# Kernel optimization log

Measured on AMD Instinct MI355X. Metric: run time of the kernel, lower is better.

## Reference

```python
import jax, jax.numpy as jnp
import numpy as np
import math

D_MODEL = 512
N_HEADS = 8
D_K = D_MODEL // N_HEADS
D_FF = 2048
EPS = 1e-6


def _layer_norm(x, gamma, beta):
    # Matches the torch module: unbiased std (ddof=1), divide by (std + eps)
    mean = jnp.mean(x, axis=-1, keepdims=True)
    std = jnp.std(x, axis=-1, ddof=1, keepdims=True)
    return gamma * (x - mean) / (std + EPS) + beta


def setup_inputs() -> dict:
    key = jax.random.key(0)
    ks = jax.random.split(key, 16)
    B, S = 4, 2048
    s_attn = 1.0 / math.sqrt(D_MODEL)
    s_ff1 = 1.0 / math.sqrt(D_MODEL)
    s_ff2 = 1.0 / math.sqrt(D_FF)
    inp = {
        "x": jax.random.normal(ks[0], (B, S, D_MODEL), dtype=jnp.float32),
        "mask": jnp.ones((1, 1, S, S), dtype=jnp.int32),
        "wq": jax.random.normal(ks[1], (D_MODEL, D_MODEL), jnp.float32) * s_attn,
        "bq": jnp.zeros((D_MODEL,), jnp.float32),
        "wk": jax.random.normal(ks[2], (D_MODEL, D_MODEL), jnp.float32) * s_attn,
        "bk": jnp.zeros((D_MODEL,), jnp.float32),
        "wv": jax.random.normal(ks[3], (D_MODEL, D_MODEL), jnp.float32) * s_attn,
        "bv": jnp.zeros((D_MODEL,), jnp.float32),
        "wo": jax.random.normal(ks[4], (D_MODEL, D_MODEL), jnp.float32) * s_attn,
        "bo": jnp.zeros((D_MODEL,), jnp.float32),
        "w1": jax.random.normal(ks[5], (D_MODEL, D_FF), jnp.float32) * s_ff1,
        "b1": jnp.zeros((D_FF,), jnp.float32),
        "w2": jax.random.normal(ks[6], (D_FF, D_MODEL), jnp.float32) * s_ff2,
        "b2": jnp.zeros((D_MODEL,), jnp.float32),
        "g1": jnp.ones((1, 1, D_MODEL), jnp.float32),
        "be1": jnp.zeros((1, 1, D_MODEL), jnp.float32),
        "g2": jnp.ones((1, 1, D_MODEL), jnp.float32),
        "be2": jnp.zeros((1, 1, D_MODEL), jnp.float32),
    }
    return inp


def reference(x, mask, wq, bq, wk, bk, wv, bv, wo, bo, w1, b1, w2, b2, g1, be1, g2, be2):
    B, S, _ = x.shape
    # --- residual 1: pre-norm self-attention ---
    xn = _layer_norm(x, g1, be1)
    q = (xn @ wq + bq).reshape(B, S, N_HEADS, D_K).transpose(0, 2, 1, 3)
    k = (xn @ wk + bk).reshape(B, S, N_HEADS, D_K).transpose(0, 2, 1, 3)
    v = (xn @ wv + bv).reshape(B, S, N_HEADS, D_K).transpose(0, 2, 1, 3)
    # NOTE: source uses floor division `//` by sqrt(d_k) (a faithful-ly kept bug)
    scores = jnp.floor_divide(jnp.einsum("bhqd,bhkd->bhqk", q, k), math.sqrt(D_K))
    scores = jnp.where(mask == 0, jnp.float32(-1e9), scores)
    attn = jax.nn.softmax(scores, axis=-1)
    ctx = jnp.einsum("bhqk,bhkd->bhqd", attn, v)
    ctx = ctx.transpose(0, 2, 1, 3).reshape(B, S, D_MODEL)
    x = x + (ctx @ wo + bo)
    # --- residual 2: pre-norm feed-forward ---
    xn2 = _layer_norm(x, g2, be2)
    ff = jax.nn.relu(xn2 @ w1 + b1) @ w2 + b2
    return x + ff
```

## Files before the change

kernel.cpp:

```cpp
#include <hip/hip_runtime.h>
#include <cmath>

#define SEQ 2048
#define DM 512
#define DFF 2048
#define NH 8
#define DKH 64
#define NROWS 8192

typedef __attribute__((ext_vector_type(8))) short bf16x8;
typedef __attribute__((ext_vector_type(16))) float f32x16;

__device__ __forceinline__ ushort f2bf(float f) {
    uint u = __float_as_uint(f);
    u += 0x7fff + ((u >> 16) & 1);
    return (ushort)(u >> 16);
}
__device__ __forceinline__ float bf2f(ushort h) {
    return __uint_as_float(((uint)h) << 16);
}
__device__ __forceinline__ uint cvtpk_bf16(float a, float b) {
    uint r;
    asm("v_cvt_pk_bf16_f32 %0, %1, %2" : "=v"(r) : "v"(a), "v"(b));
    return r;
}
__device__ __forceinline__ void gl_lds16(const void* g, void* l) {
    __builtin_amdgcn_global_load_lds(
        (const __attribute__((address_space(1))) void*)g,
        (__attribute__((address_space(3))) void*)l, 16, 0, 0);
}
__device__ __forceinline__ void* swz(char* base, int row, int col) {
    int byte = (row << 7) + (col << 1);
    byte ^= (row & 7) << 4;
    return base + byte;
}
__device__ __forceinline__ void* swzg(char* base, int row, int k) {
    int byte = (row << 7) + (k << 1);
    byte ^= ((row >> 2) & 7) << 4;
    return base + byte;
}

template<bool SPLIT>
__global__ __launch_bounds__(64) void ln_kernel(const float* __restrict__ x,
        const float* __restrict__ g, const float* __restrict__ b,
        ushort* __restrict__ oh, ushort* __restrict__ ol) {
    int row = blockIdx.x;
    int t = threadIdx.x;
    const float* xr = x + (size_t)row * DM + t * 8;
    float v[8];
    *(float4*)&v[0] = *(const float4*)(xr);
    *(float4*)&v[4] = *(const float4*)(xr + 4);
    float s = 0.f;
    #pragma unroll
    for (int j = 0; j < 8; ++j) s += v[j];
    #pragma unroll
    for (int m = 32; m > 0; m >>= 1) s += __shfl_xor(s, m);
    float mean = s * (1.0f / DM);
    float ss = 0.f;
    #pragma unroll
    for (int j = 0; j < 8; ++j) { float d = v[j] - mean; ss += d * d; }
    #pragma unroll
    for (int m = 32; m > 0; m >>= 1) ss += __shfl_xor(ss, m);
    float inv = 1.0f / (sqrtf(ss * (1.0f / (DM - 1))) + 1e-6f);
    float gv[8], bv[8];
    *(float4*)&gv[0] = *(const float4*)(g + t * 8);
    *(float4*)&gv[4] = *(const float4*)(g + t * 8 + 4);
    *(float4*)&bv[0] = *(const float4*)(b + t * 8);
    *(float4*)&bv[4] = *(const float4*)(b + t * 8 + 4);
    union { ushort us[8]; float4 f4; } ph, pl;
    #pragma unroll
    for (int j = 0; j < 8; ++j) {
        float o = gv[j] * (v[j] - mean) * inv + bv[j];
        ushort hb = f2bf(o);
        ph.us[j] = hb;
        if (SPLIT) pl.us[j] = f2bf(o - bf2f(hb));
    }
    *(float4*)(oh + (size_t)row * DM + t * 8) = ph.f4;
    if (SPLIT) *(float4*)(ol + (size_t)row * DM + t * 8) = pl.f4;
}

__global__ __launch_bounds__(256) void wconv4(
        const float* __restrict__ wq, const float* __restrict__ wk,
        const float* __restrict__ wv, const float* __restrict__ wo,
        ushort* __restrict__ qh, ushort* __restrict__ ql,
        ushort* __restrict__ kh, ushort* __restrict__ kl,
        ushort* __restrict__ vh, ushort* __restrict__ oh) {
    const int K = DM, N = DM;
    __shared__ float tile[64][65];
    int z = blockIdx.z;
    const float* W = (z == 0) ? wq : (z == 1) ? wk : (z == 2) ? wv : wo;
    ushort* Th = (z == 0) ? qh : (z == 1) ? kh : (z == 2) ? vh : oh;
    ushort* Tl = (z == 0) ? ql : (z == 1) ? kl : nullptr;
    bool split = (z < 2);
    int k0 = blockIdx.x * 64, n0 = blockIdx.y * 64;
    int t = threadIdx.x;
    {
        int kr = t >> 2, c0 = (t & 3) * 16;
        const float* src = W + (size_t)(k0 + kr) * N + n0 + c0;
        #pragma unroll
        for (int j = 0; j < 4; ++j)
            *(float4*)&tile[kr][c0 + j * 4] = *(const float4*)(src + j * 4);
    }
    __syncthreads();
    int n = t >> 2, kc = (t & 3) * 16;
    union { ushort us[16]; float4 f4[2]; } ph, pl;
    #pragma unroll
    for (int j = 0; j < 16; ++j) {
        float v = tile[kc + j][n];
        ushort hb = f2bf(v);
        ph.us[j] = hb;
        pl.us[j] = f2bf(v - bf2f(hb));
    }
    ushort* dh = Th + (size_t)(n0 + n) * K + k0 + kc;
    *(float4*)(dh) = ph.f4[0];
    *(float4*)(dh + 8) = ph.f4[1];
    if (split) {
        ushort* dl = Tl + (size_t)(n0 + n) * K + k0 + kc;
        *(float4*)(dl) = pl.f4[0];
        *(float4*)(dl + 8) = pl.f4[1];
    }
}

__global__ __launch_bounds__(256) void wconv(const float* __restrict__ W,
        ushort* __restrict__ Th, int K, int N) {
    __shared__ float tile[64][65];
    int k0 = blockIdx.x * 64, n0 = blockIdx.y * 64;
    int t = threadIdx.x;
    {
        int kr = t >> 2, c0 = (t & 3) * 16;
        const float* src = W + (size_t)(k0 + kr) * N + n0 + c0;
        #pragma unroll
        for (int j = 0; j < 4; ++j)
            *(float4*)&tile[kr][c0 + j * 4] = *(const float4*)(src + j * 4);
    }
    __syncthreads();
    int n = t >> 2, kc = (t & 3) * 16;
    union { ushort us[16]; float4 f4[2]; } ph;
    #pragma unroll
    for (int j = 0; j < 16; ++j) ph.us[j] = f2bf(tile[kc + j][n]);
    ushort* dh = Th + (size_t)(n0 + n) * K + k0 + kc;
    *(float4*)(dh) = ph.f4[0];
    *(float4*)(dh + 8) = ph.f4[1];
}

__global__ __launch_bounds__(256) void vtrans(const ushort* __restrict__ vh,
        ushort* __restrict__ vt) {
    __shared__ __align__(16) char tile[8192];
    int s0 = blockIdx.x * 64;
    int bh = blockIdx.y;
    int b = bh >> 3, h = bh & 7;
    int t = threadIdx.x;
    {
        int r = t >> 2, co = (t & 3) * 16;
        const ushort* src = vh + (size_t)(b * SEQ + s0 + r) * DM + h * DKH + co;
        *(float4*)swz(tile, r, co) = *(const float4*)(src);
        *(float4*)swz(tile, r, co + 8) = *(const float4*)(src + 8);
    }
    __syncthreads();
    int d = t >> 2, j0 = (t & 3) * 16;
    union { ushort us[16]; float4 f4[2]; } o;
    #pragma unroll
    for (int j = 0; j < 16; ++j)
        o.us[j] = *(ushort*)swz(tile, j0 + j, d);
    ushort* dst = vt + ((size_t)bh * DKH + d) * SEQ + s0 + j0;
    *(float4*)(dst) = o.f4[0];
    *(float4*)(dst + 8) = o.f4[1];
}

__global__ __launch_bounds__(64) void maskprep(const int* __restrict__ mask,
        ushort* __restrict__ mb, unsigned char* __restrict__ mflag) {
    int row = blockIdx.x;
    int lane = threadIdx.x;
    ushort neg = f2bf(-1e9f);
    unsigned long long bal[4];
    #pragma unroll
    for (int u = 0; u < 4; ++u) {
        int base = row * SEQ + u * 512 + lane * 8;
        int4 a = *(const int4*)(mask + base);
        int4 c = *(const int4*)(mask + base + 4);
        union { ushort us[8]; float4 f4; } o;
        o.us[0] = a.x ? (ushort)0 : neg;
        o.us[1] = a.y ? (ushort)0 : neg;
        o.us[2] = a.z ? (ushort)0 : neg;
        o.us[3] = a.w ? (ushort)0 : neg;
        o.us[4] = c.x ? (ushort)0 : neg;
        o.us[5] = c.y ? (ushort)0 : neg;
        o.us[6] = c.z ? (ushort)0 : neg;
        o.us[7] = c.w ? (ushort)0 : neg;
        *(float4*)(mb + base) = o.f4;
        bool ok = a.x && a.y && a.z && a.w && c.x && c.y && c.z && c.w;
        bal[u] = __ballot(ok);
    }
    if (lane < 32) {
        int u = lane >> 3;
        unsigned long long bsel = bal[0];
        bsel = (u == 1) ? bal[1] : bsel;
        bsel = (u == 2) ? bal[2] : bsel;
        bsel = (u == 3) ? bal[3] : bsel;
        int byte = (int)((bsel >> ((lane & 7) * 8)) & 0xFFull);
        mflag[row * 32 + lane] = (byte == 0xFF) ? 1 : 0;
    }
}

template<bool RELU, bool HASRES, int OUT>
__global__ __launch_bounds__(256) void mgemm(
        const ushort* __restrict__ Ah, const ushort* __restrict__ Bth,
        const float* __restrict__ bias, const float* __restrict__ resid,
        float* __restrict__ Cf, ushort* __restrict__ Cbh,
        int M, int N, int K) {
    __shared__ __align__(16) char smem[65536];
    int tid = threadIdx.x;
    int lane = tid & 63, w = tid >> 6;
    int ln31 = lane & 31, hi = lane >> 5;
    int mh = (w >> 1) * 64, nh = (w & 1) * 64;
    int gx = gridDim.x;
    int nwg = gx * gridDim.y;
    int flat = blockIdx.y * gx + blockIdx.x;
    int sid = (flat & 7) * (nwg >> 3) + (flat >> 3);
    int n0 = (sid % gx) * 128;
    int m0 = (sid / gx) * 128;

    f32x16 acc[2][2];
    #pragma unroll
    for (int i = 0; i < 2; ++i)
        #pragma unroll
        for (int j = 0; j < 2; ++j)
            #pragma unroll
            for (int r = 0; r < 16; ++r) acc[i][j][r] = 0.f;

    auto stage = [&](char* Abuf, char* Bbuf, int k0) {
        #pragma unroll
        for (int c = 0; c < 4; ++c) {
            int ch = w * 4 + c;
            int r = ch * 8 + (lane >> 3);
            int u = (lane & 7) ^ ((r >> 2) & 7);
            gl_lds16(Ah + (size_t)(m0 + r) * K + k0 + u * 8, Abuf + ch * 1024);
            gl_lds16(Bth + (size_t)(n0 + r) * K + k0 + u * 8, Bbuf + ch * 1024);
        }
    };

    char* A0 = smem;
    char* B0 = smem + 16384;
    char* A1 = smem + 32768;
    char* B1 = smem + 49152;

    stage(A0, B0, 0);
    __syncthreads();
    int nk = K / 64;
    for (int kt = 0; kt < nk; ++kt) {
        char* Ac = (kt & 1) ? A1 : A0;
        char* Bc = (kt & 1) ? B1 : B0;
        if (kt + 1 < nk)
            stage((kt & 1) ? A0 : A1, (kt & 1) ? B0 : B1, (kt + 1) * 64);
        __builtin_amdgcn_s_setprio(1);
        #pragma unroll
        for (int km = 0; km < 4; ++km) {
            int kk = km * 16 + hi * 8;
            bf16x8 ah[2], bh[2];
            ah[0] = *(bf16x8*)swzg(Ac, mh + ln31, kk);
            ah[1] = *(bf16x8*)swzg(Ac, mh + 32 + ln31, kk);
            bh[0] = *(bf16x8*)swzg(Bc, nh + ln31, kk);
            bh[1] = *(bf16x8*)swzg(Bc, nh + 32 + ln31, kk);
            #pragma unroll
            for (int mi = 0; mi < 2; ++mi)
                #pragma unroll
                for (int ni = 0; ni < 2; ++ni)
                    acc[mi][ni] = __builtin_amdgcn_mfma_f32_32x32x16_bf16(
                        ah[mi], bh[ni], acc[mi][ni], 0, 0, 0);
        }
        __builtin_amdgcn_s_setprio(0);
        __syncthreads();
    }
    float bv[2];
    bv[0] = bias[n0 + nh + ln31];
    bv[1] = bias[n0 + nh + 32 + ln31];
    #pragma unroll
    for (int mi = 0; mi < 2; ++mi)
        #pragma unroll
        for (int ni = 0; ni < 2; ++ni) {
            int n = n0 + nh + ni * 32 + ln31;
            #pragma unroll
            for (int r = 0; r < 16; ++r) {
                int m = m0 + mh + mi * 32 + (r & 3) + 8 * (r >> 2) + 4 * hi;
                float v = acc[mi][ni][r] + bv[ni];
                if (HASRES) v += resid[(size_t)m * N + n];
                if (RELU) v = fmaxf(v, 0.f);
                size_t idx = (size_t)m * N + n;
                if (OUT == 0) Cf[idx] = v;
                else Cbh[idx] = f2bf(v);
            }
        }
}

__global__ __launch_bounds__(256) void qkv_gemm(
        const ushort* __restrict__ Ah, const ushort* __restrict__ Al,
        const ushort* __restrict__ Bth, const ushort* __restrict__ Btl,
        const float* __restrict__ bq, const float* __restrict__ bk,
        const float* __restrict__ bv_, ushort* __restrict__ q_h,
        ushort* __restrict__ q_l, ushort* __restrict__ k_h,
        ushort* __restrict__ k_l, ushort* __restrict__ v_h) {
    const int K = DM, N = DM;
    __shared__ __align__(16) char smem[65536];
    char* As_h = smem;
    char* Bs_h = smem + 16384;
    char* As_l = smem + 32768;
    char* Bs_l = smem + 49152;
    int tid = threadIdx.x;
    int lane = tid & 63, w = tid >> 6;
    int ln31 = lane & 31, hi = lane >> 5;
    int mh = (w >> 1) * 64, nh = (w & 1) * 64;
    int gx = gridDim.x;
    int nwg = gx * gridDim.y;
    int flat = blockIdx.y * gx + blockIdx.x;
    int sid = (flat & 7) * (nwg >> 3) + (flat >> 3);
    int n0 = (sid % gx) * 128;
    int m0 = (sid / gx) * 128;
    bool isqk = (n0 < 1024);

    f32x16 acc[2][2];
    #pragma unroll
    for (int i = 0; i < 2; ++i)
        #pragma unroll
        for (int j = 0; j < 2; ++j)
            #pragma unroll
            for (int r = 0; r < 16; ++r) acc[i][j][r] = 0.f;

    for (int k0 = 0; k0 < K; k0 += 64) {
        #pragma unroll
        for (int c = 0; c < 4; ++c) {
            int ch = w * 4 + c;
            int r = ch * 8 + (lane >> 3);
            int u = (lane & 7) ^ ((r >> 2) & 7);
            gl_lds16(Ah + (size_t)(m0 + r) * K + k0 + u * 8, As_h + ch * 1024);
            gl_lds16(Bth + (size_t)(n0 + r) * K + k0 + u * 8, Bs_h + ch * 1024);
            if (isqk) {
                gl_lds16(Al + (size_t)(m0 + r) * K + k0 + u * 8, As_l + ch * 1024);
                gl_lds16(Btl + (size_t)(n0 + r) * K + k0 + u * 8, Bs_l + ch * 1024);
            }
        }
        __syncthreads();
        __builtin_amdgcn_s_setprio(1);
        #pragma unroll
        for (int km = 0; km < 4; ++km) {
            int kk = km * 16 + hi * 8;
            bf16x8 ah[2], bh[2];
            ah[0] = *(bf16x8*)swzg(As_h, mh + ln31, kk);
            ah[1] = *(bf16x8*)swzg(As_h, mh + 32 + ln31, kk);
            bh[0] = *(bf16x8*)swzg(Bs_h, nh + ln31, kk);
            bh[1] = *(bf16x8*)swzg(Bs_h, nh + 32 + ln31, kk);
            if (isqk) {
                bf16x8 al[2], bl[2];
                al[0] = *(bf16x8*)swzg(As_l, mh + ln31, kk);
                al[1] = *(bf16x8*)swzg(As_l, mh + 32 + ln31, kk);
                bl[0] = *(bf16x8*)swzg(Bs_l, nh + ln31, kk);
                bl[1] = *(bf16x8*)swzg(Bs_l, nh + 32 + ln31, kk);
                #pragma unroll
                for (int mi = 0; mi < 2; ++mi)
                    #pragma unroll
                    for (int ni = 0; ni < 2; ++ni) {
                        acc[mi][ni] = __builtin_amdgcn_mfma_f32_32x32x16_bf16(
                            ah[mi], bh[ni], acc[mi][ni], 0, 0, 0);
                        acc[mi][ni] = __builtin_amdgcn_mfma_f32_32x32x16_bf16(
                            ah[mi], bl[ni], acc[mi][ni], 0, 0, 0);
                        acc[mi][ni] = __builtin_amdgcn_mfma_f32_32x32x16_bf16(
                            al[mi], bh[ni], acc[mi][ni], 0, 0, 0);
                    }
            } else {
                #pragma unroll
                for (int mi = 0; mi < 2; ++mi)
                    #pragma unroll
                    for (int ni = 0; ni < 2; ++ni)
                        acc[mi][ni] = __builtin_amdgcn_mfma_f32_32x32x16_bf16(
                            ah[mi], bh[ni], acc[mi][ni], 0, 0, 0);
            }
        }
        __builtin_amdgcn_s_setprio(0);
        __syncthreads();
    }
    const float* bias = (n0 < 512) ? bq : (n0 < 1024 ? bk : bv_);
    int ncol0 = n0 & 511;
    ushort* Oh = (n0 < 512) ? q_h : (n0 < 1024 ? k_h : v_h);
    ushort* Ol = (n0 < 512) ? q_l : (n0 < 1024 ? k_l : nullptr);
    float scale = (n0 < 512) ? 0.125f : 1.0f;
    float bvv[2];
    bvv[0] = bias[ncol0 + nh + ln31];
    bvv[1] = bias[ncol0 + nh + 32 + ln31];
    #pragma unroll
    for (int mi = 0; mi < 2; ++mi)
        #pragma unroll
        for (int ni = 0; ni < 2; ++ni) {
            int n = ncol0 + nh + ni * 32 + ln31;
            #pragma unroll
            for (int r = 0; r < 16; ++r) {
                int m = m0 + mh + mi * 32 + (r & 3) + 8 * (r >> 2) + 4 * hi;
                float v = (acc[mi][ni][r] + bvv[ni]) * scale;
                size_t idx = (size_t)m * N + n;
                ushort hb = f2bf(v);
                Oh[idx] = hb;
                if (isqk) Ol[idx] = f2bf(v - bf2f(hb));
            }
        }
}

__global__ __launch_bounds__(256, 3) void attn_kernel(
        const ushort* __restrict__ Qh, const ushort* __restrict__ Ql,
        const ushort* __restrict__ Khg, const ushort* __restrict__ Klg,
        const ushort* __restrict__ Vtg, const ushort* __restrict__ mb,
        const unsigned char* __restrict__ mflag,
        ushort* __restrict__ pctx0, ushort* __restrict__ pctx1,
        float2* __restrict__ ml) {
    __shared__ __align__(16) char smem[40960];
    int tid = threadIdx.x;
    int w = tid >> 6, lane = tid & 63;
    int ln31 = lane & 31, hi = lane >> 5;
    bool hib = (hi != 0);
    int f = blockIdx.y * gridDim.x + blockIdx.x;
    int g = (f & 7) * 128 + (f >> 3);
    int bh = g >> 5, rest = g & 31;
    int part = rest >> 4, qb = rest & 15;
    int b = bh >> 3, h = bh & 7;
    int q0 = qb * 128;
    size_t brow = (size_t)b * SEQ;
    int hcol = h * DKH;
    int ktbeg = part * 16, ktend = ktbeg + 16;

    auto stage_K = [&](int kt) {
        char* buf = smem + (kt & 1) * 16384;
        #pragma unroll
        for (int c = 0; c < 2; ++c) {
            int ch = w * 2 + c;
            int r = ch * 8 + (lane >> 3);
            int u = (lane & 7) ^ (r & 7);
            gl_lds16(Khg + (brow + kt * 64 + r) * DM + hcol + u * 8,
                     buf + ch * 1024);
            gl_lds16(Klg + (brow + kt * 64 + r) * DM + hcol + u * 8,
                     buf + 8192 + ch * 1024);
        }
    };
    auto stage_V = [&](int kt) {
        char* buf = smem + 32768;
        #pragma unroll
        for (int c = 0; c < 2; ++c) {
            int ch = w * 2 + c;
            int r = ch * 8 + (lane >> 3);
            int u = (lane & 7) ^ (r & 7);
            gl_lds16(Vtg + ((size_t)bh * DKH + r) * SEQ + kt * 64 + u * 8,
                     buf + ch * 1024);
        }
    };

    {
        char* QhL = smem;
        char* QlL = smem + 16384;
        #pragma unroll
        for (int c = 0; c < 4; ++c) {
            int ch = w * 4 + c;
            int r = ch * 8 + (lane >> 3);
            int u = (lane & 7) ^ (r & 7);
            gl_lds16(Qh + (brow + q0 + r) * DM + hcol + u * 8, QhL + ch * 1024);
            gl_lds16(Ql + (brow + q0 + r) * DM + hcol + u * 8, QlL + ch * 1024);
        }
    }
    __syncthreads();
    bf16x8 qfh[4], qfl[4];
    {
        int qr = w * 32 + ln31;
        #pragma unroll
        for (int c = 0; c < 4; ++c) {
            qfh[c] = *(bf16x8*)swz(smem, qr, c * 16 + hi * 8);
            qfl[c] = *(bf16x8*)swz(smem + 16384, qr, c * 16 + hi * 8);
        }
    }
    __syncthreads();
    stage_K(ktbeg);
    stage_V(ktbeg);
    __syncthreads();

    f32x16 ctx0, ctx1;
    #pragma unroll
    for (int r = 0; r < 16; ++r) { ctx0[r] = 0.f; ctx1[r] = 0.f; }
    float m_i = -1e30f, l_i = 0.f;
    int qglob = q0 + w * 32 + ln31;
    const ushort* mrow = mb + (size_t)qglob * SEQ;

    for (int kt = ktbeg; kt < ktend; ++kt) {
        if (kt + 1 < ktend) stage_K(kt + 1);
        char* KhL = smem + (kt & 1) * 16384;
        char* KlL = KhL + 8192;
        char* VtL = smem + 32768;
        unsigned char fl = mflag[qglob * 32 + kt];
        bool domask = !__all(fl != 0);
        ushort4 mpre[8];
        if (domask) {
            #pragma unroll
            for (int i = 0; i < 8; ++i)
                mpre[i] = *(const ushort4*)(mrow + kt * 64 + i * 8 + hi * 4);
        }
        #pragma unroll
        for (int ksub = 0; ksub < 2; ++ksub) {
            f32x16 s;
            #pragma unroll
            for (int r = 0; r < 16; ++r) s[r] = 0.f;
            __builtin_amdgcn_s_setprio(1);
            #pragma unroll
            for (int c = 0; c < 4; ++c) {
                bf16x8 ka = *(bf16x8*)swz(KhL, ksub * 32 + ln31, c * 16 + hi * 8);
                bf16x8 kb = *(bf16x8*)swz(KlL, ksub * 32 + ln31, c * 16 + hi * 8);
                s = __builtin_amdgcn_mfma_f32_32x32x16_bf16(ka, qfh[c], s, 0, 0, 0);
                s = __builtin_amdgcn_mfma_f32_32x32x16_bf16(ka, qfl[c], s, 0, 0, 0);
                s = __builtin_amdgcn_mfma_f32_32x32x16_bf16(kb, qfh[c], s, 0, 0, 0);
            }
            __builtin_amdgcn_s_setprio(0);
            float tmax = -1e30f;
            if (domask) {
                #pragma unroll
                for (int rg = 0; rg < 4; ++rg) {
                    ushort4 mv = mpre[ksub * 4 + rg];
                    ushort mu[4] = {mv.x, mv.y, mv.z, mv.w};
                    #pragma unroll
                    for (int j = 0; j < 4; ++j) {
                        int r = rg * 4 + j;
                        float sc = floorf(s[r]) + bf2f(mu[j]);
                        s[r] = sc;
                        tmax = fmaxf(tmax, sc);
                    }
                }
            } else {
                #pragma unroll
                for (int r = 0; r < 16; ++r) {
                    float sc = floorf(s[r]);
                    s[r] = sc;
                    tmax = fmaxf(tmax, sc);
                }
            }
            tmax = fmaxf(tmax, __shfl_xor(tmax, 32));
            if (!__all(tmax <= m_i)) {
                float newm = fmaxf(m_i, tmax);
                float scl = __expf(m_i - newm);
                m_i = newm;
                l_i *= scl;
                #pragma unroll
                for (int r = 0; r < 16; ++r) { ctx0[r] *= scl; ctx1[r] *= scl; }
            }
            float psum = 0.f;
            #pragma unroll
            for (int r = 0; r < 16; ++r) {
                float p = __expf(s[r] - m_i);
                s[r] = p;
                psum += p;
            }
            psum += __shfl_xor(psum, 32);
            l_i += psum;
            uint pk0[4], pk1[4];
            #pragma unroll
            for (int rg = 0; rg < 4; ++rg) {
                pk0[rg] = cvtpk_bf16(s[rg * 4 + 0], s[rg * 4 + 1]);
                pk1[rg] = cvtpk_bf16(s[rg * 4 + 2], s[rg * 4 + 3]);
            }
            bf16x8 pb[2];
            #pragma unroll
            for (int cc = 0; cc < 2; ++cc) {
                uint A0 = pk0[cc * 2], A1 = pk1[cc * 2];
                uint B0 = pk0[cc * 2 + 1], B1 = pk1[cc * 2 + 1];
                uint send0 = hib ? A0 : B0;
                uint send1 = hib ? A1 : B1;
                uint own0  = hib ? B0 : A0;
                uint own1  = hib ? B1 : A1;
                uint recv0 = (uint)__shfl_xor((int)send0, 32);
                uint recv1 = (uint)__shfl_xor((int)send1, 32);
                union { uint u[4]; bf16x8 v; } pbu;
                pbu.u[0] = hib ? recv0 : own0;
                pbu.u[1] = hib ? recv1 : own1;
                pbu.u[2] = hib ? own0 : recv0;
                pbu.u[3] = hib ? own1 : recv1;
                pb[cc] = pbu.v;
            }
            if (ksub == 0) __syncthreads();
            __builtin_amdgcn_s_setprio(1);
            #pragma unroll
            for (int cc = 0; cc < 2; ++cc) {
                int c = ksub * 2 + cc;
                bf16x8 va0 = *(bf16x8*)swz(VtL, ln31, c * 16 + hi * 8);
                bf16x8 va1 = *(bf16x8*)swz(VtL, 32 + ln31, c * 16 + hi * 8);
                ctx0 = __builtin_amdgcn_mfma_f32_32x32x16_bf16(va0, pb[cc], ctx0, 0, 0, 0);
                ctx1 = __builtin_amdgcn_mfma_f32_32x32x16_bf16(va1, pb[cc], ctx1, 0, 0, 0);
            }
            __builtin_amdgcn_s_setprio(0);
        }
        __syncthreads();
        if (kt + 1 < ktend) stage_V(kt + 1);
    }

    ushort* P = part ? pctx1 : pctx0;
    size_t pbase = ((size_t)bh * SEQ + qglob) * DKH;
    #pragma unroll
    for (int r = 0; r < 16; ++r) {
        int d = (r & 3) + 8 * (r >> 2) + 4 * hi;
        P[pbase + d] = f2bf(ctx0[r]);
        P[pbase + 32 + d] = f2bf(ctx1[r]);
    }
    if (hi == 0)
        ml[((size_t)part * 32 + bh) * SEQ + qglob] = make_float2(m_i, l_i);
}

__global__ __launch_bounds__(256) void attn_combine(
        const ushort* __restrict__ p0, const ushort* __restrict__ p1,
        const float2* __restrict__ ml, ushort* __restrict__ O) {
    int idx = blockIdx.x * 256 + threadIdx.x;
    int d0 = (idx & 7) * 8;
    int q = (idx >> 3) & (SEQ - 1);
    int bh = idx >> 14;
    int b = bh >> 3, h = bh & 7;
    size_t pb = ((size_t)bh * SEQ + q) * DKH + d0;
    bf16x8 c0 = *(const bf16x8*)(p0 + pb);
    bf16x8 c1 = *(const bf16x8*)(p1 + pb);
    float2 e0 = ml[(size_t)bh * SEQ + q];
    float2 e1 = ml[((size_t)32 + bh) * SEQ + q];
    float m = fmaxf(e0.x, e1.x);
    float w0 = __expf(e0.x - m), w1 = __expf(e1.x - m);
    float inv = 1.0f / (e0.y * w0 + e1.y * w1);
    union { ushort us[8]; float4 f4; } o;
    #pragma unroll
    for (int j = 0; j < 8; ++j) {
        float v0 = bf2f((ushort)c0[j]);
        float v1 = bf2f((ushort)c1[j]);
        o.us[j] = f2bf((v0 * w0 + v1 * w1) * inv);
    }
    *(float4*)(O + ((size_t)(b * SEQ + q)) * DM + h * DKH + d0) = o.f4;
}

extern "C" void kernel_launch(void* const* d_in, const int* in_sizes, int n_in,
                              void* d_out, int out_size, void* d_ws, size_t ws_size,
                              hipStream_t stream) {
    const float* x    = (const float*)d_in[0];
    const int*   mask = (const int*)d_in[1];
    const float* wq = (const float*)d_in[2];
    const float* bq = (const float*)d_in[3];
    const float* wk = (const float*)d_in[4];
    const float* bk = (const float*)d_in[5];
    const float* wv = (const float*)d_in[6];
    const float* bv = (const float*)d_in[7];
    const float* wo = (const float*)d_in[8];
    const float* bo = (const float*)d_in[9];
    const float* w1 = (const float*)d_in[10];
    const float* b1 = (const float*)d_in[11];
    const float* w2 = (const float*)d_in[12];
    const float* b2 = (const float*)d_in[13];
    const float* g1  = (const float*)d_in[14];
    const float* be1 = (const float*)d_in[15];
    const float* g2  = (const float*)d_in[16];
    const float* be2 = (const float*)d_in[17];
    float* out = (float*)d_out;

    char* ws = (char*)d_ws;
    const size_t MiB = 1024 * 1024;
    ushort* xn_h = (ushort*)(ws);
    ushort* xn_l = (ushort*)(ws + 8 * MiB);
    ushort* q_h  = (ushort*)(ws + 16 * MiB);
    ushort* q_l  = (ushort*)(ws + 24 * MiB);
    ushort* k_h  = (ushort*)(ws + 32 * MiB);
    ushort* k_l  = (ushort*)(ws + 40 * MiB);
    ushort* v_h  = (ushort*)(ws + 48 * MiB);
    ushort* v_t  = (ushort*)(ws + 56 * MiB);
    ushort* wqkvt_h = (ushort*)(ws + 64 * MiB);
    ushort* wqkvt_l = (ushort*)(ws + 66 * MiB);
    ushort* wot_h = (ushort*)(ws + 67 * MiB);
    unsigned char* mflag = (unsigned char*)(ws + 67 * MiB + 512 * 1024);
    ushort* w1t_h = (ushort*)(ws + 68 * MiB);
    ushort* w2t_h = (ushort*)(ws + 70 * MiB);
    ushort* mb    = (ushort*)(ws + 72 * MiB);
    ushort* pctx0 = (ushort*)(ws + 80 * MiB);
    ushort* pctx1 = (ushort*)(ws + 88 * MiB);
    float2* ml    = (float2*)(ws + 64 * MiB);
    ushort* ctx  = xn_h;
    ushort* xn2  = xn_l;
    ushort* ff1  = q_h;

    dim3 blk256(256);
    wconv4<<<dim3(8, 8, 4), blk256, 0, stream>>>(
        wq, wk, wv, wo, wqkvt_h, wqkvt_l, wqkvt_h + 512 * 512,
        wqkvt_l + 512 * 512, wqkvt_h + 1024 * 512, wot_h);
    wconv<<<dim3(8, 32), blk256, 0, stream>>>(w1, w1t_h, DM, DFF);
    wconv<<<dim3(32, 8), blk256, 0, stream>>>(w2, w2t_h, DFF, DM);
    maskprep<<<SEQ, 64, 0, stream>>>(mask, mb, mflag);
    ln_kernel<true><<<NROWS, 64, 0, stream>>>(x, g1, be1, xn_h, xn_l);
    qkv_gemm<<<dim3(12, NROWS / 128), blk256, 0, stream>>>(
        xn_h, xn_l, wqkvt_h, wqkvt_l, bq, bk, bv, q_h, q_l, k_h, k_l, v_h);
    vtrans<<<dim3(SEQ / 64, 4 * NH), blk256, 0, stream>>>(v_h, v_t);
    {
        dim3 grid(32, 32);
        attn_kernel<<<grid, blk256, 0, stream>>>(
            q_h, q_l, k_h, k_l, v_t, mb, mflag, pctx0, pctx1, ml);
    }
    attn_combine<<<32 * SEQ * 8 / 256, blk256, 0, stream>>>(pctx0, pctx1, ml, ctx);
    {
        dim3 grid(DM / 128, NROWS / 128);
        mgemm<false,true,0><<<grid, blk256, 0, stream>>>(
            ctx, wot_h, bo, x, out, nullptr, NROWS, DM, DM);
    }
    ln_kernel<false><<<NROWS, 64, 0, stream>>>(out, g2, be2, xn2, nullptr);
    {
        dim3 grid(DFF / 128, NROWS / 128);
        mgemm<true,false,1><<<grid, blk256, 0, stream>>>(
            xn2, w1t_h, b1, nullptr, nullptr, ff1, NROWS, DFF, DM);
    }
    {
        dim3 grid(DM / 128, NROWS / 128);
        mgemm<false,true,0><<<grid, blk256, 0, stream>>>(
            ff1, w2t_h, b2, out, out, nullptr, NROWS, DM, DFF);
    }
}
```

Measured before the change: 247.9 us.

## Fuse prep kernels, widen layernorm blocks, single-buffer attention K/V for occupancy

Merges the four weight-conversion and mask-prep launches into one prep kernel to cut launch overhead, and runs layernorm with four rows per 256-thread block instead of one row per 64-thread block. The attention kernel drops K double-buffering and the separate V buffer in favour of a single shared stage of K-high, K-low and V per tile. This shrinks LDS from 40KB to 32KB so launch bounds can allow 4 blocks per CU instead of 3, at the cost of losing overlap between loads and compute. It also moves the ml buffer to its own workspace offset, since it previously shared an offset with the weight buffers.

```diff
diff --git a/kernel.cpp b/kernel.cpp
--- a/kernel.cpp
+++ b/kernel.cpp
@@ -41,11 +41,11 @@
 }
 
 template<bool SPLIT>
-__global__ __launch_bounds__(64) void ln_kernel(const float* __restrict__ x,
+__global__ __launch_bounds__(256) void ln_kernel(const float* __restrict__ x,
         const float* __restrict__ g, const float* __restrict__ b,
         ushort* __restrict__ oh, ushort* __restrict__ ol) {
-    int row = blockIdx.x;
-    int t = threadIdx.x;
+    int row = blockIdx.x * 4 + (threadIdx.x >> 6);
+    int t = threadIdx.x & 63;
     const float* xr = x + (size_t)row * DM + t * 8;
     float v[8];
     *(float4*)&v[0] = *(const float4*)(xr);
@@ -79,68 +79,100 @@
     if (SPLIT) *(float4*)(ol + (size_t)row * DM + t * 8) = pl.f4;
 }
 
-__global__ __launch_bounds__(256) void wconv4(
+__global__ __launch_bounds__(256) void prep(
         const float* __restrict__ wq, const float* __restrict__ wk,
         const float* __restrict__ wv, const float* __restrict__ wo,
+        const float* __restrict__ w1, const float* __restrict__ w2,
+        const int* __restrict__ mask,
         ushort* __restrict__ qh, ushort* __restrict__ ql,
         ushort* __restrict__ kh, ushort* __restrict__ kl,
-        ushort* __restrict__ vh, ushort* __restrict__ oh) {
-    const int K = DM, N = DM;
+        ushort* __restrict__ vh, ushort* __restrict__ oh,
+        ushort* __restrict__ w1t, ushort* __restrict__ w2t,
+        ushort* __restrict__ mb, unsigned char* __restrict__ mflag) {
     __shared__ float tile[64][65];
-    int z = blockIdx.z;
-    const float* W = (z == 0) ? wq : (z == 1) ? wk : (z == 2) ? wv : wo;
-    ushort* Th = (z == 0) ? qh : (z == 1) ? kh : (z == 2) ? vh : oh;
-    ushort* Tl = (z == 0) ? ql : (z == 1) ? kl : nullptr;
-    bool split = (z < 2);
-    int k0 = blockIdx.x * 64, n0 = blockIdx.y * 64;
+    int id = blockIdx.x;
     int t = threadIdx.x;
-    {
-        int kr = t >> 2, c0 = (t & 3) * 16;
-        const float* src = W + (size_t)(k0 + kr) * N + n0 + c0;
-        #pragma unroll
-        for (int j = 0; j < 4; ++j)
-            *(float4*)&tile[kr][c0 + j * 4] = *(const float4*)(src + j * 4);
-    }
-    __syncthreads();
-    int n = t >> 2, kc = (t & 3) * 16;
-    union { ushort us[16]; float4 f4[2]; } ph, pl;
-    #pragma unroll
-    for (int j = 0; j < 16; ++j) {
-        float v = tile[kc + j][n];
-        ushort hb = f2bf(v);
-        ph.us[j] = hb;
-        pl.us[j] = f2bf(v - bf2f(hb));
-    }
-    ushort* dh = Th + (size_t)(n0 + n) * K + k0 + kc;
-    *(float4*)(dh) = ph.f4[0];
-    *(float4*)(dh + 8) = ph.f4[1];
-    if (split) {
-        ushort* dl = Tl + (size_t)(n0 + n) * K + k0 + kc;
-        *(float4*)(dl) = pl.f4[0];
-        *(float4*)(dl + 8) = pl.f4[1];
-    }
-}
-
-__global__ __launch_bounds__(256) void wconv(const float* __restrict__ W,
-        ushort* __restrict__ Th, int K, int N) {
-    __shared__ float tile[64][65];
-    int k0 = blockIdx.x * 64, n0 = blockIdx.y * 64;
-    int t = threadIdx.x;
-    {
-        int kr = t >> 2, c0 = (t & 3) * 16;
-        const float* src = W + (size_t)(k0 + kr) * N + n0 + c0;
-        #pragma unroll
-        for (int j = 0; j < 4; ++j)
-            *(float4*)&tile[kr][c0 + j * 4] = *(const float4*)(src + j * 4);
-    }
-    __syncthreads();
-    int n = t >> 2, kc = (t & 3) * 16;
-    union { ushort us[16]; float4 f4[2]; } ph;
-    #pragma unroll
-    for (int j = 0; j < 16; ++j) ph.us[j] = f2bf(tile[kc + j][n]);
-    ushort* dh = Th + (size_t)(n0 + n) * K + k0 + kc;
-    *(float4*)(dh) = ph.f4[0];
-    *(float4*)(dh + 8) = ph.f4[1];
+    if (id < 768) {
+        const float* W;
+        ushort* Th;
+        ushort* Tl = nullptr;
+        int K, N, k0, n0;
+        bool split = false;
+        if (id < 256) {
+            int z = id >> 6, r = id & 63;
+            W = (z == 0) ? wq : (z == 1) ? wk : (z == 2) ? wv : wo;
+            Th = (z == 0) ? qh : (z == 1) ? kh : (z == 2) ? vh : oh;
+            Tl = (z == 0) ? ql : (z == 1) ? kl : nullptr;
+            split = (z < 2);
+            K = DM; N = DM;
+            k0 = (r >> 3) * 64; n0 = (r & 7) * 64;
+        } else if (id < 512) {
+            int r = id - 256;
+            W = w1; Th = w1t; K = DM; N = DFF;
+            k0 = (r & 7) * 64; n0 = (r >> 3) * 64;
+        } else {
+            int r = id - 512;
+            W = w2; Th = w2t; K = DFF; N = DM;
+            k0 = (r & 31) * 64; n0 = (r >> 5) * 64;
+        }
+        {
+            int kr = t >> 2, c0 = (t & 3) * 16;
+            const float* src = W + (size_t)(k0 + kr) * N + n0 + c0;
+            #pragma unroll
+            for (int j = 0; j < 4; ++j)
+                *(float4*)&tile[kr][c0 + j * 4] = *(const float4*)(src + j * 4);
+        }
+        __syncthreads();
+        int n = t >> 2, kc = (t & 3) * 16;
+        union { ushort us[16]; float4 f4[2]; } ph, pl;
+        #pragma unroll
+        for (int j = 0; j < 16; ++j) {
+            float v = tile[kc + j][n];
+            ushort hb = f2bf(v);
+            ph.us[j] = hb;
+            pl.us[j] = f2bf(v - bf2f(hb));
+        }
+        ushort* dh = Th + (size_t)(n0 + n) * K + k0 + kc;
+        *(float4*)(dh) = ph.f4[0];
+        *(float4*)(dh + 8) = ph.f4[1];
+        if (split) {
+            ushort* dl = Tl + (size_t)(n0 + n) * K + k0 + kc;
+            *(float4*)(dl) = pl.f4[0];
+            *(float4*)(dl + 8) = pl.f4[1];
+        }
+    } else {
+        int row = (id - 768) * 4 + (t >> 6);
+        int lane = t & 63;
+        ushort neg = f2bf(-1e9f);
+        unsigned long long bal[4];
+        #pragma unroll
+        for (int u = 0; u < 4; ++u) {
+            int base = row * SEQ + u * 512 + lane * 8;
+            int4 a = *(const int4*)(mask + base);
+            int4 c = *(const int4*)(mask + base + 4);
+            union { ushort us[8]; float4 f4; } o;
+            o.us[0] = a.x ? (ushort)0 : neg;
+            o.us[1] = a.y ? (ushort)0 : neg;
+            o.us[2] = a.z ? (ushort)0 : neg;
+            o.us[3] = a.w ? (ushort)0 : neg;
+            o.us[4] = c.x ? (ushort)0 : neg;
+            o.us[5] = c.y ? (ushort)0 : neg;
+            o.us[6] = c.z ? (ushort)0 : neg;
+            o.us[7] = c.w ? (ushort)0 : neg;
+            *(float4*)(mb + base) = o.f4;
+            bool ok = a.x && a.y && a.z && a.w && c.x && c.y && c.z && c.w;
+            bal[u] = __ballot(ok);
+        }
+        if (lane < 32) {
+            int u = lane >> 3;
+            unsigned long long bsel = bal[0];
+            bsel = (u == 1) ? bal[1] : bsel;
+            bsel = (u == 2) ? bal[2] : bsel;
+            bsel = (u == 3) ? bal[3] : bsel;
+            int byte = (int)((bsel >> ((lane & 7) * 8)) & 0xFFull);
+            mflag[row * 32 + lane] = (byte == 0xFF) ? 1 : 0;
+        }
+    }
 }
 
 __global__ __launch_bounds__(256) void vtrans(const ushort* __restrict__ vh,
@@ -165,41 +197,6 @@
     ushort* dst = vt + ((size_t)bh * DKH + d) * SEQ + s0 + j0;
     *(float4*)(dst) = o.f4[0];
     *(float4*)(dst + 8) = o.f4[1];
-}
-
-__global__ __launch_bounds__(64) void maskprep(const int* __restrict__ mask,
-        ushort* __restrict__ mb, unsigned char* __restrict__ mflag) {
-    int row = blockIdx.x;
-    int lane = threadIdx.x;
-    ushort neg = f2bf(-1e9f);
-    unsigned long long bal[4];
-    #pragma unroll
-    for (int u = 0; u < 4; ++u) {
-        int base = row * SEQ + u * 512 + lane * 8;
-        int4 a = *(const int4*)(mask + base);
-        int4 c = *(const int4*)(mask + base + 4);
-        union { ushort us[8]; float4 f4; } o;
-        o.us[0] = a.x ? (ushort)0 : neg;
-        o.us[1] = a.y ? (ushort)0 : neg;
-        o.us[2] = a.z ? (ushort)0 : neg;
-        o.us[3] = a.w ? (ushort)0 : neg;
-        o.us[4] = c.x ? (ushort)0 : neg;
-        o.us[5] = c.y ? (ushort)0 : neg;
-        o.us[6] = c.z ? (ushort)0 : neg;
-        o.us[7] = c.w ? (ushort)0 : neg;
-        *(float4*)(mb + base) = o.f4;
-        bool ok = a.x && a.y && a.z && a.w && c.x && c.y && c.z && c.w;
-        bal[u] = __ballot(ok);
-    }
-    if (lane < 32) {
-        int u = lane >> 3;
-        unsigned long long bsel = bal[0];
-        bsel = (u == 1) ? bal[1] : bsel;
-        bsel = (u == 2) ? bal[2] : bsel;
-        bsel = (u == 3) ? bal[3] : bsel;
-        int byte = (int)((bsel >> ((lane & 7) * 8)) & 0xFFull);
-        mflag[row * 32 + lane] = (byte == 0xFF) ? 1 : 0;
-    }
 }
 
 template<bool RELU, bool HASRES, int OUT>
@@ -402,14 +399,14 @@
         }
 }
 
-__global__ __launch_bounds__(256, 3) void attn_kernel(
+__global__ __launch_bounds__(256, 4) void attn_kernel(
         const ushort* __restrict__ Qh, const ushort* __restrict__ Ql,
         const ushort* __restrict__ Khg, const ushort* __restrict__ Klg,
         const ushort* __restrict__ Vtg, const ushort* __restrict__ mb,
         const unsigned char* __restrict__ mflag,
         ushort* __restrict__ pctx0, ushort* __restrict__ pctx1,
         float2* __restrict__ ml) {
-    __shared__ __align__(16) char smem[40960];
+    __shared__ __align__(16) char smem[32768];
     int tid = threadIdx.x;
     int w = tid >> 6, lane = tid & 63;
     int ln31 = lane & 31, hi = lane >> 5;
@@ -424,28 +421,18 @@
     int hcol = h * DKH;
     int ktbeg = part * 16, ktend = ktbeg + 16;
 
-    auto stage_K = [&](int kt) {
-        char* buf = smem + (kt & 1) * 16384;
+    auto stage_kv = [&](int kt) {
         #pragma unroll
         for (int c = 0; c < 2; ++c) {
             int ch = w * 2 + c;
             int r = ch * 8 + (lane >> 3);
             int u = (lane & 7) ^ (r & 7);
             gl_lds16(Khg + (brow + kt * 64 + r) * DM + hcol + u * 8,
-                     buf + ch * 1024);
+                     smem + ch * 1024);
             gl_lds16(Klg + (brow + kt * 64 + r) * DM + hcol + u * 8,
-                     buf + 8192 + ch * 1024);
-        }
-    };
-    auto stage_V = [&](int kt) {
-        char* buf = smem + 32768;
-        #pragma unroll
-        for (int c = 0; c < 2; ++c) {
-            int ch = w * 2 + c;
-            int r = ch * 8 + (lane >> 3);
-            int u = (lane & 7) ^ (r & 7);
+                     smem + 8192 + ch * 1024);
             gl_lds16(Vtg + ((size_t)bh * DKH + r) * SEQ + kt * 64 + u * 8,
-                     buf + ch * 1024);
+                     smem + 16384 + ch * 1024);
         }
     };
 
@@ -472,9 +459,6 @@
         }
     }
     __syncthreads();
-    stage_K(ktbeg);
-    stage_V(ktbeg);
-    __syncthreads();
 
     f32x16 ctx0, ctx1;
     #pragma unroll
@@ -484,10 +468,7 @@
     const ushort* mrow = mb + (size_t)qglob * SEQ;
 
     for (int kt = ktbeg; kt < ktend; ++kt) {
-        if (kt + 1 < ktend) stage_K(kt + 1);
-        char* KhL = smem + (kt & 1) * 16384;
-        char* KlL = KhL + 8192;
-        char* VtL = smem + 32768;
+        stage_kv(kt);
         unsigned char fl = mflag[qglob * 32 + kt];
         bool domask = !__all(fl != 0);
         ushort4 mpre[8];
@@ -496,6 +477,10 @@
             for (int i = 0; i < 8; ++i)
                 mpre[i] = *(const ushort4*)(mrow + kt * 64 + i * 8 + hi * 4);
         }
+        __syncthreads();
+        char* KhL = smem;
+        char* KlL = smem + 8192;
+        char* VtL = smem + 16384;
         #pragma unroll
         for (int ksub = 0; ksub < 2; ++ksub) {
             f32x16 s;
@@ -575,7 +560,6 @@
                 pbu.u[3] = hib ? own1 : recv1;
                 pb[cc] = pbu.v;
             }
-            if (ksub == 0) __syncthreads();
             __builtin_amdgcn_s_setprio(1);
             #pragma unroll
             for (int cc = 0; cc < 2; ++cc) {
@@ -588,7 +572,6 @@
             __builtin_amdgcn_s_setprio(0);
         }
         __syncthreads();
-        if (kt + 1 < ktend) stage_V(kt + 1);
     }
 
     ushort* P = part ? pctx1 : pctx0;
@@ -671,19 +654,17 @@
     ushort* mb    = (ushort*)(ws + 72 * MiB);
     ushort* pctx0 = (ushort*)(ws + 80 * MiB);
     ushort* pctx1 = (ushort*)(ws + 88 * MiB);
-    float2* ml    = (float2*)(ws + 64 * MiB);
+    float2* ml    = (float2*)(ws + 96 * MiB);
     ushort* ctx  = xn_h;
     ushort* xn2  = xn_l;
     ushort* ff1  = q_h;
 
     dim3 blk256(256);
-    wconv4<<<dim3(8, 8, 4), blk256, 0, stream>>>(
-        wq, wk, wv, wo, wqkvt_h, wqkvt_l, wqkvt_h + 512 * 512,
-        wqkvt_l + 512 * 512, wqkvt_h + 1024 * 512, wot_h);
-    wconv<<<dim3(8, 32), blk256, 0, stream>>>(w1, w1t_h, DM, DFF);
-    wconv<<<dim3(32, 8), blk256, 0, stream>>>(w2, w2t_h, DFF, DM);
-    maskprep<<<SEQ, 64, 0, stream>>>(mask, mb, mflag);
-    ln_kernel<true><<<NROWS, 64, 0, stream>>>(x, g1, be1, xn_h, xn_l);
+    prep<<<1280, blk256, 0, stream>>>(
+        wq, wk, wv, wo, w1, w2, mask,
+        wqkvt_h, wqkvt_l, wqkvt_h + 512 * 512, wqkvt_l + 512 * 512,
+        wqkvt_h + 1024 * 512, wot_h, w1t_h, w2t_h, mb, mflag);
+    ln_kernel<true><<<NROWS / 4, blk256, 0, stream>>>(x, g1, be1, xn_h, xn_l);
     qkv_gemm<<<dim3(12, NROWS / 128), blk256, 0, stream>>>(
         xn_h, xn_l, wqkvt_h, wqkvt_l, bq, bk, bv, q_h, q_l, k_h, k_l, v_h);
     vtrans<<<dim3(SEQ / 64, 4 * NH), blk256, 0, stream>>>(v_h, v_t);
@@ -698,7 +679,7 @@
         mgemm<false,true,0><<<grid, blk256, 0, stream>>>(
             ctx, wot_h, bo, x, out, nullptr, NROWS, DM, DM);
     }
-    ln_kernel<false><<<NROWS, 64, 0, stream>>>(out, g2, be2, xn2, nullptr);
+    ln_kernel<false><<<NROWS / 4, blk256, 0, stream>>>(out, g2, be2, xn2, nullptr);
     {
         dim3 grid(DFF / 128, NROWS / 128);
         mgemm<true,false,1><<<grid, blk256, 0, stream>>>(
```

Result: slower. 279.0 us (+12.6%).
